# Performance work log

Measured on AMD Instinct MI355X. Metric: run time of the kernel, lower is better.

## Reference

```python
import jax, jax.numpy as jnp
import numpy as np

NUM_NODES = 100000
NODE_DIM = 64
MEM_DIM = 64
EMBED = 64   # out_channels
HEADS = 2
IN_DIM = NODE_DIM + MEM_DIM  # 128
N = 50000    # batch nodes (len(n_id))
E = 800000   # edges in local subgraph


def setup_inputs() -> dict:
    key = jax.random.key(0)
    ks = jax.random.split(key, 12)
    s = 1.0 / np.sqrt(IN_DIM)
    inp = {
        "n_id": jax.random.randint(ks[0], (N,), 0, NUM_NODES),
        "edge_index": jax.random.randint(ks[1], (2, E), 0, N),
        # non-learned TGN memory state (detached in forward)
        "memory_table": jax.random.normal(ks[2], (NUM_NODES, MEM_DIM), jnp.float32),
        # learned node embedding table
        "emb_table": jax.random.normal(ks[3], (NUM_NODES, NODE_DIM), jnp.float32),
        # TransformerConv linear layers; weights stored [in, out] so y = x @ W + b
        "Wq": jax.random.normal(ks[4], (IN_DIM, HEADS * EMBED), jnp.float32) * s,
        "bq": jnp.zeros((HEADS * EMBED,), jnp.float32),
        "Wk": jax.random.normal(ks[5], (IN_DIM, HEADS * EMBED), jnp.float32) * s,
        "bk": jnp.zeros((HEADS * EMBED,), jnp.float32),
        "Wv": jax.random.normal(ks[6], (IN_DIM, HEADS * EMBED), jnp.float32) * s,
        "bv": jnp.zeros((HEADS * EMBED,), jnp.float32),
        "Wskip": jax.random.normal(ks[7], (IN_DIM, EMBED), jnp.float32) * s,
        "bskip": jnp.zeros((EMBED,), jnp.float32),
    }
    return inp


def reference(n_id, edge_index, memory_table, emb_table, Wq, bq, Wk, bk, Wv, bv, Wskip, bskip):
    # memory lookup (detached) + embedding lookup + concat([emb, mem])
    z = jax.lax.stop_gradient(memory_table[n_id])          # [N, MEM_DIM]
    x = jnp.concatenate([emb_table[n_id], z], axis=-1)     # [N, IN_DIM]

    q = (x @ Wq + bq).reshape(N, HEADS, EMBED)
    k = (x @ Wk + bk).reshape(N, HEADS, EMBED)
    v = (x @ Wv + bv).reshape(N, HEADS, EMBED)

    src, dst = edge_index[0], edge_index[1]
    # per-edge attention score: (q_i . k_j) / sqrt(d), i = dst, j = src
    score = jnp.einsum("ehd,ehd->eh", q[dst], k[src]) / np.sqrt(EMBED)  # [E, H]
    # scatter-softmax over incoming edges of each destination node
    smax = jax.ops.segment_max(score, dst, num_segments=N)              # [N, H]
    exps = jnp.exp(score - smax[dst])                                   # [E, H]
    denom = jax.ops.segment_sum(exps, dst, num_segments=N)              # [N, H]
    alpha = exps / denom[dst]                                           # [E, H]

    msg = alpha[:, :, None] * v[src]                                    # [E, H, D]
    out = jax.ops.segment_sum(msg, dst, num_segments=N)                 # [N, H, D]
    out = out.mean(axis=1)                                              # concat=False -> mean over heads
    out = out + x @ Wskip + bskip                                       # root_weight skip
    return out
```

## Files before the change

kernel.cpp:

```cpp
#include <hip/hip_runtime.h>
#include <math.h>


typedef unsigned int uint32;
typedef unsigned short ushort16;
typedef __attribute__((ext_vector_type(8))) short short8;
typedef __attribute__((ext_vector_type(4))) float floatx4;

__device__ __forceinline__ ushort16 f2bf(float f) {
  union { float f; uint32 u; } x; x.f = f;
  uint32 r = x.u + 0x7fffu + ((x.u >> 16) & 1u);
  return (ushort16)(r >> 16);
}
__device__ __forceinline__ float bf_lo(uint32 u) {
  union { uint32 u; float f; } x; x.u = u << 16; return x.f;
}
__device__ __forceinline__ float bf_hi(uint32 u) {
  union { uint32 u; float f; } x; x.u = u & 0xffff0000u; return x.f;
}
__device__ __forceinline__ void unpack8(uint4 u, float* f) {
  f[0] = bf_lo(u.x); f[1] = bf_hi(u.x); f[2] = bf_lo(u.y); f[3] = bf_hi(u.y);
  f[4] = bf_lo(u.z); f[5] = bf_hi(u.z); f[6] = bf_lo(u.w); f[7] = bf_hi(u.w);
}
__device__ __forceinline__ short8 pack8s(float4 a, float4 b) {
  union { uint32 u[4]; short8 s; } r;
  r.u[0] = (uint32)f2bf(a.x) | ((uint32)f2bf(a.y) << 16);
  r.u[1] = (uint32)f2bf(a.z) | ((uint32)f2bf(a.w) << 16);
  r.u[2] = (uint32)f2bf(b.x) | ((uint32)f2bf(b.y) << 16);
  r.u[3] = (uint32)f2bf(b.z) | ((uint32)f2bf(b.w) << 16);
  return r.s;
}

__global__ __launch_bounds__(256) void prep_hist_kernel(
    const float* __restrict__ Wq, const float* __restrict__ bq,
    const float* __restrict__ Wk, const float* __restrict__ bk,
    const float* __restrict__ Wv, const float* __restrict__ bv,
    const float* __restrict__ Ws, const float* __restrict__ bs,
    ushort16* __restrict__ Wt, float* __restrict__ ball,
    const int* __restrict__ dstA, int E, int* __restrict__ counts) {
  int idx = blockIdx.x * 256 + threadIdx.x;
  if (idx < 448 * 128) {
    int n = idx >> 7, k = idx & 127;
    float w;
    if (n < 128)      w = Wq[k * 128 + n];
    else if (n < 256) w = Wk[k * 128 + (n - 128)];
    else if (n < 384) w = Wv[k * 128 + (n - 256)];
    else              w = Ws[k * 64 + (n - 384)];
    Wt[idx] = f2bf(w);
  }
  if (idx < 448) {
    float b;
    if (idx < 128)      b = bq[idx];
    else if (idx < 256) b = bk[idx - 128];
    else if (idx < 384) b = bv[idx - 256];
    else                b = bs[idx - 384];
    ball[idx] = b;
  }
  if (idx < E) atomicAdd(&counts[dstA[idx]], 1);
}

__global__ __launch_bounds__(256) void scan1_kernel(const int* __restrict__ counts,
                                                    int* __restrict__ offs,
                                                    int* __restrict__ bsum, int N) {
  __shared__ int s[256];
  int b = blockIdx.x, t = threadIdx.x;
  int base = b * 4096 + t * 16;
  int vals[16];
  int sum = 0;
#pragma unroll
  for (int i = 0; i < 16; ++i) {
    int idx = base + i;
    vals[i] = (idx < N) ? counts[idx] : 0;
    sum += vals[i];
  }
  s[t] = sum;
  __syncthreads();
  for (int off = 1; off < 256; off <<= 1) {
    int vv = (t >= off) ? s[t - off] : 0;
    __syncthreads();
    s[t] += vv;
    __syncthreads();
  }
  int run = (t > 0) ? s[t - 1] : 0;
#pragma unroll
  for (int i = 0; i < 16; ++i) {
    int idx = base + i;
    if (idx < N) offs[idx] = run;
    run += vals[i];
  }
  if (t == 255) bsum[b] = s[255];
}

__global__ __launch_bounds__(256) void scan3_kernel(int* __restrict__ offs,
                                                    const int* __restrict__ bsum,
                                                    int* __restrict__ cursor,
                                                    int N, int E) {
  int i = blockIdx.x * blockDim.x + threadIdx.x;
  if (i < N) {
    int blk = i >> 12;
    int add = 0;
    for (int j = 0; j < blk; ++j) add += bsum[j];
    int v = offs[i] + add;
    offs[i] = v;
    cursor[i] = v;
  }
  if (i == 0) offs[N] = E;
}

__global__ __launch_bounds__(256) void scatter_kernel(
    const int* __restrict__ srcA, const int* __restrict__ dstA, int E,
    int* __restrict__ cursor, int* __restrict__ sorted_src) {
  int e = blockIdx.x * blockDim.x + threadIdx.x;
  if (e < E) {
    int d = dstA[e];
    int p = atomicAdd(&cursor[d], 1);
    sorted_src[p] = srcA[e];
  }
}

#define LDB 136
__global__ __launch_bounds__(256) void qkv_mfma2_kernel(
    const int* __restrict__ n_id, const float* __restrict__ embtab,
    const float* __restrict__ memtab,
    const ushort16* __restrict__ Wt, const float* __restrict__ ball,
    ushort16* __restrict__ qb, ushort16* __restrict__ kb, ushort16* __restrict__ vb,
    float* __restrict__ outskip, int N) {
  __shared__ ushort16 Bs[2][64 * LDB];
  int t = threadIdx.x;
  int wave = t >> 6, lane = t & 63;
  int lrow = lane & 15, quad = lane >> 4;
  int grow = blockIdx.x * 64 + wave * 16 + lrow;
  bool rvalid = grow < N;
  int srcrow = rvalid ? n_id[grow] : 0;

  const float* embp = embtab + (size_t)srcrow * 64 + quad * 8;
  const float* memp = memtab + (size_t)srcrow * 64 + quad * 8;
  short8 af[4];
  af[0] = pack8s(*(const float4*)(embp), *(const float4*)(embp + 4));
  af[1] = pack8s(*(const float4*)(embp + 32), *(const float4*)(embp + 36));
  af[2] = pack8s(*(const float4*)(memp), *(const float4*)(memp + 4));
  af[3] = pack8s(*(const float4*)(memp + 32), *(const float4*)(memp + 36));

  int sr[4], sc[4];
  uint4 breg[4];
#pragma unroll
  for (int rep = 0; rep < 4; ++rep) {
    int idx = rep * 256 + t;
    sr[rep] = idx >> 4;
    sc[rep] = (idx & 15) * 8;
    breg[rep] = *(const uint4*)(Wt + (size_t)sr[rep] * 128 + sc[rep]);
  }
#pragma unroll
  for (int rep = 0; rep < 4; ++rep)
    *(uint4*)&Bs[0][sr[rep] * LDB + sc[rep]] = breg[rep];
  __syncthreads();

  for (int ct = 0; ct < 7; ++ct) {
    int buf = ct & 1;
    if (ct < 6) {
      const ushort16* wp = Wt + (size_t)(ct + 1) * 8192;
#pragma unroll
      for (int rep = 0; rep < 4; ++rep)
        breg[rep] = *(const uint4*)(wp + (size_t)sr[rep] * 128 + sc[rep]);
    }

    floatx4 acc[4];
#pragma unroll
    for (int j = 0; j < 4; ++j) acc[j] = (floatx4)(0.f);

#pragma unroll
    for (int kk = 0; kk < 4; ++kk) {
      int koff = kk * 32 + quad * 8;
#pragma unroll
      for (int jt = 0; jt < 4; ++jt) {
        short8 bf = *(const short8*)&Bs[buf][(jt * 16 + lrow) * LDB + koff];
        acc[jt] = __builtin_amdgcn_mfma_f32_16x16x32_bf16(bf, af[kk], acc[jt], 0, 0, 0);
      }
    }

    if (rvalid) {
      int col0 = ct * 64;
#pragma unroll
      for (int jt = 0; jt < 4; ++jt) {
        int gcol = col0 + jt * 16 + quad * 4;
        float4 bias = *(const float4*)(ball + gcol);
        float o0 = acc[jt][0] + bias.x;
        float o1 = acc[jt][1] + bias.y;
        float o2 = acc[jt][2] + bias.z;
        float o3 = acc[jt][3] + bias.w;
        if (ct < 6) {
          uint2 pk;
          pk.x = (uint32)f2bf(o0) | ((uint32)f2bf(o1) << 16);
          pk.y = (uint32)f2bf(o2) | ((uint32)f2bf(o3) << 16);
          if (ct < 2)      *(uint2*)(qb + (size_t)grow * 128 + gcol)         = pk;
          else if (ct < 4) *(uint2*)(kb + (size_t)grow * 128 + (gcol - 128)) = pk;
          else             *(uint2*)(vb + (size_t)grow * 128 + (gcol - 256)) = pk;
        } else {
          *(float4*)(outskip + (size_t)grow * 64 + (gcol - 384)) =
              make_float4(o0, o1, o2, o3);
        }
      }
    }

    if (ct < 6) {
#pragma unroll
      for (int rep = 0; rep < 4; ++rep)
        *(uint4*)&Bs[buf ^ 1][sr[rep] * LDB + sc[rep]] = breg[rep];
      __syncthreads();
    }
  }
}

#define EXPC 0.1803368801111244f
__global__ __launch_bounds__(256) void attn_kernel(
    const ushort16* __restrict__ qb, const ushort16* __restrict__ kb,
    const ushort16* __restrict__ vb, const int* __restrict__ offs,
    const int* __restrict__ ssrc, float* __restrict__ out, int N) {
  int tid = threadIdx.x;
  int wave = tid >> 6, lane = tid & 63;
  int nsub = lane >> 4;
  int l16 = lane & 15;
  int head = l16 >> 3;
  int l8 = lane & 7;
  int node = (blockIdx.x * 4 + wave) * 4 + nsub;
  bool valid = node < N;
  int nodeC = valid ? node : 0;

  int e0 = 0, e1 = 0;
  if (valid) { e0 = offs[node]; e1 = offs[node + 1]; }
  int deg = e1 - e0;
  int md = deg;
  md = max(md, __shfl_xor(md, 16));
  md = max(md, __shfl_xor(md, 32));

  int hoff = head * 64 + l8 * 8;
  float qf[8];
  {
    uint4 qu = *(const uint4*)(qb + (size_t)nodeC * 128 + hoff);
    unpack8(qu, qf);
  }

  float l = 0.f;
  float a[8];
#pragma unroll
  for (int j = 0; j < 8; ++j) a[j] = 0.f;

  uint4 k0v = make_uint4(0, 0, 0, 0), v0v = k0v, k1v = k0v, v1v = k0v;
  if (md > 0) {
    int e = e0;
    int s = (e < e1) ? ssrc[e] : 0;
    k0v = *(const uint4*)(kb + (size_t)s * 128 + hoff);
    v0v = *(const uint4*)(vb + (size_t)s * 128 + hoff);
  }
  if (md > 1) {
    int e = e0 + 1;
    int s = (e < e1) ? ssrc[e] : 0;
    k1v = *(const uint4*)(kb + (size_t)s * 128 + hoff);
    v1v = *(const uint4*)(vb + (size_t)s * 128 + hoff);
  }

  for (int i = 0; i < md; ++i) {
    uint4 kc = k0v, vc = v0v;
    k0v = k1v; v0v = v1v;
    if (i + 2 < md) {
      int e = e0 + i + 2;
      int s = (e < e1) ? ssrc[e] : 0;
      k1v = *(const uint4*)(kb + (size_t)s * 128 + hoff);
      v1v = *(const uint4*)(vb + (size_t)s * 128 + hoff);
    }
    float kf[8], vf[8];
    unpack8(kc, kf);
    unpack8(vc, vf);
    float p = qf[0] * kf[0];
#pragma unroll
    for (int j = 1; j < 8; ++j) p = fmaf(qf[j], kf[j], p);
    p += __shfl_xor(p, 1);
    p += __shfl_xor(p, 2);
    p += __shfl_xor(p, 4);
    float w = (i < deg) ? exp2f(p * EXPC) : 0.f;
    l += w;
#pragma unroll
    for (int j = 0; j < 8; ++j) a[j] = fmaf(w, vf[j], a[j]);
  }

  float inv = (l > 0.f) ? 0.5f / l : 0.f;
  float r[8];
#pragma unroll
  for (int j = 0; j < 8; ++j) r[j] = a[j] * inv;
#pragma unroll
  for (int j = 0; j < 8; ++j) r[j] += __shfl_xor(r[j], 8);

  if (valid && head == 0) {
    float* op = out + (size_t)node * 64 + l8 * 8;
    float4 c0 = *(float4*)op;
    float4 c1 = *(float4*)(op + 4);
    c0.x += r[0]; c0.y += r[1]; c0.z += r[2]; c0.w += r[3];
    c1.x += r[4]; c1.y += r[5]; c1.z += r[6]; c1.w += r[7];
    *(float4*)op = c0;
    *(float4*)(op + 4) = c1;
  }
}

extern "C" void kernel_launch(void* const* d_in, const int* in_sizes, int n_in,
                              void* d_out, int out_size, void* d_ws, size_t ws_size,
                              hipStream_t stream) {
  const int* n_id = (const int*)d_in[0];
  const int* eidx = (const int*)d_in[1];
  const float* memtab = (const float*)d_in[2];
  const float* embtab = (const float*)d_in[3];
  const float* Wq = (const float*)d_in[4];
  const float* bq = (const float*)d_in[5];
  const float* Wk = (const float*)d_in[6];
  const float* bk = (const float*)d_in[7];
  const float* Wv = (const float*)d_in[8];
  const float* bv = (const float*)d_in[9];
  const float* Wskip = (const float*)d_in[10];
  const float* bskip = (const float*)d_in[11];

  int N = in_sizes[0];
  int E = in_sizes[1] / 2;
  const int* srcA = eidx;
  const int* dstA = eidx + E;
  float* out = (float*)d_out;

  char* w = (char*)d_ws;
  ushort16* qb = (ushort16*)w; w += (size_t)N * 128 * 2;
  ushort16* kb = (ushort16*)w; w += (size_t)N * 128 * 2;
  ushort16* vb = (ushort16*)w; w += (size_t)N * 128 * 2;
  ushort16* Wt = (ushort16*)w; w += (size_t)448 * 128 * 2;
  float* ball = (float*)w;     w += (size_t)448 * 4;
  int* counts = (int*)w;       w += (size_t)N * 4;
  int* cursor = (int*)w;       w += (size_t)N * 4;
  int* offs = (int*)w;         w += (size_t)(N + 1) * 4;
  int* bsum = (int*)w;         w += (size_t)1024 * 4;
  int* ssrc = (int*)w;         w += (size_t)E * 4;

  hipMemsetAsync(counts, 0, (size_t)N * 4, stream);

  int k1_threads = (448 * 128 > E) ? 448 * 128 : E;
  prep_hist_kernel<<<(k1_threads + 255) / 256, 256, 0, stream>>>(
      Wq, bq, Wk, bk, Wv, bv, Wskip, bskip, Wt, ball, dstA, E, counts);

  int NB = (N + 4095) / 4096;
  scan1_kernel<<<NB, 256, 0, stream>>>(counts, offs, bsum, N);
  scan3_kernel<<<(N + 255) / 256, 256, 0, stream>>>(offs, bsum, cursor, N, E);

  scatter_kernel<<<(E + 255) / 256, 256, 0, stream>>>(srcA, dstA, E, cursor, ssrc);

  qkv_mfma2_kernel<<<(N + 63) / 64, 256, 0, stream>>>(
      n_id, embtab, memtab, Wt, ball, qb, kb, vb, out, N);

  attn_kernel<<<(N + 15) / 16, 256, 0, stream>>>(qb, kb, vb, offs, ssrc, out, N);
}
```

Measured before the change: 286.0 us.

## Record atomic slot in histogram, fuse scatter and offset fix-up into QKV kernel

The histogram pass now stores each edge's atomic slot, so the CSR scatter no longer needs a second atomic pass over a cursor array. The scan fix-up and scatter blocks are merged into the QKV GEMM launch as extra blocks, which removes two kernel launches and lets the scatter overlap with the matmul. The attention loop is also unrolled to handle two edges per iteration with a deeper prefetch of four. The cost is an extra E-sized pos buffer written and read, and more registers in the attention kernel.

Result: faster. 258.6 us (-9.6%).

```diff
diff --git a/kernel.cpp b/kernel.cpp
--- a/kernel.cpp
+++ b/kernel.cpp
@@ -37,7 +37,8 @@
     const float* __restrict__ Wv, const float* __restrict__ bv,
     const float* __restrict__ Ws, const float* __restrict__ bs,
     ushort16* __restrict__ Wt, float* __restrict__ ball,
-    const int* __restrict__ dstA, int E, int* __restrict__ counts) {
+    const int* __restrict__ dstA, int E, int* __restrict__ counts,
+    int* __restrict__ pos) {
   int idx = blockIdx.x * 256 + threadIdx.x;
   if (idx < 448 * 128) {
     int n = idx >> 7, k = idx & 127;
@@ -56,11 +57,11 @@
     else                b = bs[idx - 384];
     ball[idx] = b;
   }
-  if (idx < E) atomicAdd(&counts[dstA[idx]], 1);
+  if (idx < E) pos[idx] = atomicAdd(&counts[dstA[idx]], 1);
 }
 
 __global__ __launch_bounds__(256) void scan1_kernel(const int* __restrict__ counts,
-                                                    int* __restrict__ offs,
+                                                    int* __restrict__ poffs,
                                                     int* __restrict__ bsum, int N) {
   __shared__ int s[256];
   int b = blockIdx.x, t = threadIdx.x;
@@ -85,51 +86,53 @@
 #pragma unroll
   for (int i = 0; i < 16; ++i) {
     int idx = base + i;
-    if (idx < N) offs[idx] = run;
+    if (idx < N) poffs[idx] = run;
     run += vals[i];
   }
   if (t == 255) bsum[b] = s[255];
 }
 
-__global__ __launch_bounds__(256) void scan3_kernel(int* __restrict__ offs,
-                                                    const int* __restrict__ bsum,
-                                                    int* __restrict__ cursor,
-                                                    int N, int E) {
-  int i = blockIdx.x * blockDim.x + threadIdx.x;
-  if (i < N) {
-    int blk = i >> 12;
-    int add = 0;
-    for (int j = 0; j < blk; ++j) add += bsum[j];
-    int v = offs[i] + add;
-    offs[i] = v;
-    cursor[i] = v;
-  }
-  if (i == 0) offs[N] = E;
-}
-
-__global__ __launch_bounds__(256) void scatter_kernel(
-    const int* __restrict__ srcA, const int* __restrict__ dstA, int E,
-    int* __restrict__ cursor, int* __restrict__ sorted_src) {
-  int e = blockIdx.x * blockDim.x + threadIdx.x;
-  if (e < E) {
-    int d = dstA[e];
-    int p = atomicAdd(&cursor[d], 1);
-    sorted_src[p] = srcA[e];
-  }
-}
-
 #define LDB 136
-__global__ __launch_bounds__(256) void qkv_mfma2_kernel(
+__global__ __launch_bounds__(256) void fused_kernel(
     const int* __restrict__ n_id, const float* __restrict__ embtab,
     const float* __restrict__ memtab,
     const ushort16* __restrict__ Wt, const float* __restrict__ ball,
     ushort16* __restrict__ qb, ushort16* __restrict__ kb, ushort16* __restrict__ vb,
-    float* __restrict__ outskip, int N) {
+    float* __restrict__ outskip, int N,
+    const int* __restrict__ srcA, const int* __restrict__ dstA, int E,
+    const int* __restrict__ poffs, const int* __restrict__ bsum,
+    const int* __restrict__ pos, int* __restrict__ ssrc, int* __restrict__ offs,
+    int QB, int PB) {
   __shared__ ushort16 Bs[2][64 * LDB];
+  int b = blockIdx.x;
   int t = threadIdx.x;
+
+  if (b >= QB) {
+    if (b < QB + PB) {
+      int e = (b - QB) * 256 + t;
+      if (e < E) {
+        int d = dstA[e];
+        int blk = d >> 12;
+        int add = 0;
+        for (int j = 0; j < blk; ++j) add += bsum[j];
+        ssrc[poffs[d] + add + pos[e]] = srcA[e];
+      }
+    } else {
+      int i = (b - QB - PB) * 256 + t;
+      if (i < N) {
+        int blk = i >> 12;
+        int add = 0;
+        for (int j = 0; j < blk; ++j) add += bsum[j];
+        offs[i] = poffs[i] + add;
+      }
+      if (i == 0) offs[N] = E;
+    }
+    return;
+  }
+
   int wave = t >> 6, lane = t & 63;
   int lrow = lane & 15, quad = lane >> 4;
-  int grow = blockIdx.x * 64 + wave * 16 + lrow;
+  int grow = b * 64 + wave * 16 + lrow;
   bool rvalid = grow < N;
   int srcrow = rvalid ? n_id[grow] : 0;
 
@@ -245,42 +248,57 @@
 #pragma unroll
   for (int j = 0; j < 8; ++j) a[j] = 0.f;
 
-  uint4 k0v = make_uint4(0, 0, 0, 0), v0v = k0v, k1v = k0v, v1v = k0v;
-  if (md > 0) {
-    int e = e0;
+  uint4 kr[4], vr[4];
+#pragma unroll
+  for (int j = 0; j < 4; ++j) {
+    int e = e0 + j;
     int s = (e < e1) ? ssrc[e] : 0;
-    k0v = *(const uint4*)(kb + (size_t)s * 128 + hoff);
-    v0v = *(const uint4*)(vb + (size_t)s * 128 + hoff);
-  }
-  if (md > 1) {
-    int e = e0 + 1;
-    int s = (e < e1) ? ssrc[e] : 0;
-    k1v = *(const uint4*)(kb + (size_t)s * 128 + hoff);
-    v1v = *(const uint4*)(vb + (size_t)s * 128 + hoff);
-  }
-
-  for (int i = 0; i < md; ++i) {
-    uint4 kc = k0v, vc = v0v;
-    k0v = k1v; v0v = v1v;
-    if (i + 2 < md) {
-      int e = e0 + i + 2;
+    kr[j] = (j < md) ? *(const uint4*)(kb + (size_t)s * 128 + hoff) : make_uint4(0,0,0,0);
+    vr[j] = (j < md) ? *(const uint4*)(vb + (size_t)s * 128 + hoff) : make_uint4(0,0,0,0);
+  }
+
+  for (int i = 0; i < md; i += 2) {
+    uint4 kc0 = kr[0], vc0 = vr[0], kc1 = kr[1], vc1 = vr[1];
+    kr[0] = kr[2]; vr[0] = vr[2]; kr[1] = kr[3]; vr[1] = vr[3];
+    if (i + 4 < md) {
+      int e = e0 + i + 4;
       int s = (e < e1) ? ssrc[e] : 0;
-      k1v = *(const uint4*)(kb + (size_t)s * 128 + hoff);
-      v1v = *(const uint4*)(vb + (size_t)s * 128 + hoff);
-    }
-    float kf[8], vf[8];
-    unpack8(kc, kf);
-    unpack8(vc, vf);
-    float p = qf[0] * kf[0];
-#pragma unroll
-    for (int j = 1; j < 8; ++j) p = fmaf(qf[j], kf[j], p);
-    p += __shfl_xor(p, 1);
-    p += __shfl_xor(p, 2);
-    p += __shfl_xor(p, 4);
-    float w = (i < deg) ? exp2f(p * EXPC) : 0.f;
-    l += w;
-#pragma unroll
-    for (int j = 0; j < 8; ++j) a[j] = fmaf(w, vf[j], a[j]);
+      kr[2] = *(const uint4*)(kb + (size_t)s * 128 + hoff);
+      vr[2] = *(const uint4*)(vb + (size_t)s * 128 + hoff);
+    }
+    if (i + 5 < md) {
+      int e = e0 + i + 5;
+      int s = (e < e1) ? ssrc[e] : 0;
+      kr[3] = *(const uint4*)(kb + (size_t)s * 128 + hoff);
+      vr[3] = *(const uint4*)(vb + (size_t)s * 128 + hoff);
+    }
+
+    float kf0[8], vf0[8], kf1[8], vf1[8];
+    unpack8(kc0, kf0);
+    unpack8(vc0, vf0);
+    unpack8(kc1, kf1);
+    unpack8(vc1, vf1);
+    float p0 = qf[0] * kf0[0];
+    float p1 = qf[0] * kf1[0];
+#pragma unroll
+    for (int j = 1; j < 8; ++j) {
+      p0 = fmaf(qf[j], kf0[j], p0);
+      p1 = fmaf(qf[j], kf1[j], p1);
+    }
+    p0 += __shfl_xor(p0, 1);
+    p1 += __shfl_xor(p1, 1);
+    p0 += __shfl_xor(p0, 2);
+    p1 += __shfl_xor(p1, 2);
+    p0 += __shfl_xor(p0, 4);
+    p1 += __shfl_xor(p1, 4);
+    float w0 = (i < deg) ? exp2f(p0 * EXPC) : 0.f;
+    float w1 = (i + 1 < deg) ? exp2f(p1 * EXPC) : 0.f;
+    l += w0 + w1;
+#pragma unroll
+    for (int j = 0; j < 8; ++j) {
+      a[j] = fmaf(w0, vf0[j], a[j]);
+      a[j] = fmaf(w1, vf1[j], a[j]);
+    }
   }
 
   float inv = (l > 0.f) ? 0.5f / l : 0.f;
@@ -330,25 +348,27 @@
   ushort16* Wt = (ushort16*)w; w += (size_t)448 * 128 * 2;
   float* ball = (float*)w;     w += (size_t)448 * 4;
   int* counts = (int*)w;       w += (size_t)N * 4;
-  int* cursor = (int*)w;       w += (size_t)N * 4;
+  int* poffs = (int*)w;        w += (size_t)N * 4;
   int* offs = (int*)w;         w += (size_t)(N + 1) * 4;
   int* bsum = (int*)w;         w += (size_t)1024 * 4;
   int* ssrc = (int*)w;         w += (size_t)E * 4;
+  int* pos = (int*)w;          w += (size_t)E * 4;
 
   hipMemsetAsync(counts, 0, (size_t)N * 4, stream);
 
   int k1_threads = (448 * 128 > E) ? 448 * 128 : E;
   prep_hist_kernel<<<(k1_threads + 255) / 256, 256, 0, stream>>>(
-      Wq, bq, Wk, bk, Wv, bv, Wskip, bskip, Wt, ball, dstA, E, counts);
+      Wq, bq, Wk, bk, Wv, bv, Wskip, bskip, Wt, ball, dstA, E, counts, pos);
 
   int NB = (N + 4095) / 4096;
-  scan1_kernel<<<NB, 256, 0, stream>>>(counts, offs, bsum, N);
-  scan3_kernel<<<(N + 255) / 256, 256, 0, stream>>>(offs, bsum, cursor, N, E);
-
-  scatter_kernel<<<(E + 255) / 256, 256, 0, stream>>>(srcA, dstA, E, cursor, ssrc);
-
-  qkv_mfma2_kernel<<<(N + 63) / 64, 256, 0, stream>>>(
-      n_id, embtab, memtab, Wt, ball, qb, kb, vb, out, N);
+  scan1_kernel<<<NB, 256, 0, stream>>>(counts, poffs, bsum, N);
+
+  int QB = (N + 63) / 64;
+  int PB = (E + 255) / 256;
+  int FB = (N + 255) / 256;
+  fused_kernel<<<QB + PB + FB, 256, 0, stream>>>(
+      n_id, embtab, memtab, Wt, ball, qb, kb, vb, out, N,
+      srcA, dstA, E, poffs, bsum, pos, ssrc, offs, QB, PB);
 
   attn_kernel<<<(N + 15) / 16, 256, 0, stream>>>(qb, kb, vb, offs, ssrc, out, N);
 }
```

## Fuse CSR build into QKV kernel and degree-sort attention node order

Applied to the files above, without the earlier changes.

The histogram pass now records each edge's slot from its atomicAdd, so the scatter needs no second atomic cursor pass. The scan-fixup, scatter and a new degree-bucketing pass are merged into the QKV GEMM launch as extra block ranges, which cuts kernel launches and lets the independent work overlap. The attention kernel visits nodes in degree-sorted order so that the four nodes sharing a wavefront have similar edge counts and less divergence. In exchange it adds pos and norder buffers and gives up node locality when writing the output.

New measurement: 361.0 us. 26.2% more time.

```diff
diff --git a/kernel.cpp b/kernel.cpp
--- a/kernel.cpp
+++ b/kernel.cpp
@@ -37,7 +37,8 @@
     const float* __restrict__ Wv, const float* __restrict__ bv,
     const float* __restrict__ Ws, const float* __restrict__ bs,
     ushort16* __restrict__ Wt, float* __restrict__ ball,
-    const int* __restrict__ dstA, int E, int* __restrict__ counts) {
+    const int* __restrict__ dstA, int E, int* __restrict__ counts,
+    int* __restrict__ pos) {
   int idx = blockIdx.x * 256 + threadIdx.x;
   if (idx < 448 * 128) {
     int n = idx >> 7, k = idx & 127;
@@ -56,12 +57,14 @@
     else                b = bs[idx - 384];
     ball[idx] = b;
   }
-  if (idx < E) atomicAdd(&counts[dstA[idx]], 1);
+  if (idx < E) pos[idx] = atomicAdd(&counts[dstA[idx]], 1);
 }
 
 __global__ __launch_bounds__(256) void scan1_kernel(const int* __restrict__ counts,
-                                                    int* __restrict__ offs,
-                                                    int* __restrict__ bsum, int N) {
+                                                    int* __restrict__ poffs,
+                                                    int* __restrict__ bsum,
+                                                    int* __restrict__ dcnt,
+                                                    int* __restrict__ pos2, int N) {
   __shared__ int s[256];
   int b = blockIdx.x, t = threadIdx.x;
   int base = b * 4096 + t * 16;
@@ -72,6 +75,10 @@
     int idx = base + i;
     vals[i] = (idx < N) ? counts[idx] : 0;
     sum += vals[i];
+    if (idx < N) {
+      int bin = vals[i] < 63 ? vals[i] : 63;
+      pos2[idx] = atomicAdd(&dcnt[bin], 1);
+    }
   }
   s[t] = sum;
   __syncthreads();
@@ -85,51 +92,67 @@
 #pragma unroll
   for (int i = 0; i < 16; ++i) {
     int idx = base + i;
-    if (idx < N) offs[idx] = run;
+    if (idx < N) poffs[idx] = run;
     run += vals[i];
   }
   if (t == 255) bsum[b] = s[255];
 }
 
-__global__ __launch_bounds__(256) void scan3_kernel(int* __restrict__ offs,
-                                                    const int* __restrict__ bsum,
-                                                    int* __restrict__ cursor,
-                                                    int N, int E) {
-  int i = blockIdx.x * blockDim.x + threadIdx.x;
-  if (i < N) {
-    int blk = i >> 12;
-    int add = 0;
-    for (int j = 0; j < blk; ++j) add += bsum[j];
-    int v = offs[i] + add;
-    offs[i] = v;
-    cursor[i] = v;
-  }
-  if (i == 0) offs[N] = E;
-}
-
-__global__ __launch_bounds__(256) void scatter_kernel(
-    const int* __restrict__ srcA, const int* __restrict__ dstA, int E,
-    int* __restrict__ cursor, int* __restrict__ sorted_src) {
-  int e = blockIdx.x * blockDim.x + threadIdx.x;
-  if (e < E) {
-    int d = dstA[e];
-    int p = atomicAdd(&cursor[d], 1);
-    sorted_src[p] = srcA[e];
-  }
-}
-
 #define LDB 136
-__global__ __launch_bounds__(256) void qkv_mfma2_kernel(
+__global__ __launch_bounds__(256) void fused_kernel(
     const int* __restrict__ n_id, const float* __restrict__ embtab,
     const float* __restrict__ memtab,
     const ushort16* __restrict__ Wt, const float* __restrict__ ball,
     ushort16* __restrict__ qb, ushort16* __restrict__ kb, ushort16* __restrict__ vb,
-    float* __restrict__ outskip, int N) {
+    float* __restrict__ outskip, int N,
+    const int* __restrict__ srcA, const int* __restrict__ dstA, int E,
+    const int* __restrict__ poffs, const int* __restrict__ bsum,
+    const int* __restrict__ pos, int* __restrict__ ssrc, int* __restrict__ offs,
+    const int* __restrict__ counts, const int* __restrict__ dcnt,
+    const int* __restrict__ pos2, int* __restrict__ norder,
+    int QB, int PB, int FB) {
   __shared__ ushort16 Bs[2][64 * LDB];
+  int b = blockIdx.x;
   int t = threadIdx.x;
+
+  if (b >= QB) {
+    if (b < QB + PB) {
+      int e = (b - QB) * 256 + t;
+      if (e < E) {
+        int d = dstA[e];
+        int blk = d >> 12;
+        int add = 0;
+        for (int j = 0; j < blk; ++j) add += bsum[j];
+        ssrc[poffs[d] + add + pos[e]] = srcA[e];
+      }
+    } else if (b < QB + PB + FB) {
+      int i = (b - QB - PB) * 256 + t;
+      if (i < N) {
+        int blk = i >> 12;
+        int add = 0;
+        for (int j = 0; j < blk; ++j) add += bsum[j];
+        offs[i] = poffs[i] + add;
+      }
+      if (i == 0) offs[N] = E;
+    } else {
+      __shared__ int dls[64];
+      if (t < 64) dls[t] = dcnt[t];
+      __syncthreads();
+      int i = (b - QB - PB - FB) * 256 + t;
+      if (i < N) {
+        int deg = counts[i];
+        int bin = deg < 63 ? deg : 63;
+        int dbase = 0;
+        for (int j = 0; j < bin; ++j) dbase += dls[j];
+        norder[dbase + pos2[i]] = i;
+      }
+    }
+    return;
+  }
+
   int wave = t >> 6, lane = t & 63;
   int lrow = lane & 15, quad = lane >> 4;
-  int grow = blockIdx.x * 64 + wave * 16 + lrow;
+  int grow = b * 64 + wave * 16 + lrow;
   bool rvalid = grow < N;
   int srcrow = rvalid ? n_id[grow] : 0;
 
@@ -215,16 +238,17 @@
 __global__ __launch_bounds__(256) void attn_kernel(
     const ushort16* __restrict__ qb, const ushort16* __restrict__ kb,
     const ushort16* __restrict__ vb, const int* __restrict__ offs,
-    const int* __restrict__ ssrc, float* __restrict__ out, int N) {
+    const int* __restrict__ ssrc, const int* __restrict__ norder,
+    float* __restrict__ out, int N) {
   int tid = threadIdx.x;
   int wave = tid >> 6, lane = tid & 63;
   int nsub = lane >> 4;
   int l16 = lane & 15;
   int head = l16 >> 3;
   int l8 = lane & 7;
-  int node = (blockIdx.x * 4 + wave) * 4 + nsub;
-  bool valid = node < N;
-  int nodeC = valid ? node : 0;
+  int sidx = (blockIdx.x * 4 + wave) * 4 + nsub;
+  bool valid = sidx < N;
+  int node = valid ? norder[sidx] : 0;
 
   int e0 = 0, e1 = 0;
   if (valid) { e0 = offs[node]; e1 = offs[node + 1]; }
@@ -236,7 +260,7 @@
   int hoff = head * 64 + l8 * 8;
   float qf[8];
   {
-    uint4 qu = *(const uint4*)(qb + (size_t)nodeC * 128 + hoff);
+    uint4 qu = *(const uint4*)(qb + (size_t)node * 128 + hoff);
     unpack8(qu, qf);
   }
 
@@ -330,25 +354,32 @@
   ushort16* Wt = (ushort16*)w; w += (size_t)448 * 128 * 2;
   float* ball = (float*)w;     w += (size_t)448 * 4;
   int* counts = (int*)w;       w += (size_t)N * 4;
-  int* cursor = (int*)w;       w += (size_t)N * 4;
+  int* dcnt = (int*)w;         w += (size_t)64 * 4;
+  int* poffs = (int*)w;        w += (size_t)N * 4;
   int* offs = (int*)w;         w += (size_t)(N + 1) * 4;
   int* bsum = (int*)w;         w += (size_t)1024 * 4;
   int* ssrc = (int*)w;         w += (size_t)E * 4;
-
-  hipMemsetAsync(counts, 0, (size_t)N * 4, stream);
+  int* pos = (int*)w;          w += (size_t)E * 4;
+  int* pos2 = (int*)w;         w += (size_t)N * 4;
+  int* norder = (int*)w;       w += (size_t)N * 4;
+
+  hipMemsetAsync(counts, 0, (size_t)(N + 64) * 4, stream);
 
   int k1_threads = (448 * 128 > E) ? 448 * 128 : E;
   prep_hist_kernel<<<(k1_threads + 255) / 256, 256, 0, stream>>>(
-      Wq, bq, Wk, bk, Wv, bv, Wskip, bskip, Wt, ball, dstA, E, counts);
+      Wq, bq, Wk, bk, Wv, bv, Wskip, bskip, Wt, ball, dstA, E, counts, pos);
 
   int NB = (N + 4095) / 4096;
-  scan1_kernel<<<NB, 256, 0, stream>>>(counts, offs, bsum, N);
-  scan3_kernel<<<(N + 255) / 256, 256, 0, stream>>>(offs, bsum, cursor, N, E);
-
-  scatter_kernel<<<(E + 255) / 256, 256, 0, stream>>>(srcA, dstA, E, cursor, ssrc);
-
-  qkv_mfma2_kernel<<<(N + 63) / 64, 256, 0, stream>>>(
-      n_id, embtab, memtab, Wt, ball, qb, kb, vb, out, N);
-
-  attn_kernel<<<(N + 15) / 16, 256, 0, stream>>>(qb, kb, vb, offs, ssrc, out, N);
-}
+  scan1_kernel<<<NB, 256, 0, stream>>>(counts, poffs, bsum, dcnt, pos2, N);
+
+  int QB = (N + 63) / 64;
+  int PB = (E + 255) / 256;
+  int FB = (N + 255) / 256;
+  int OB = (N + 255) / 256;
+  fused_kernel<<<QB + PB + FB + OB, 256, 0, stream>>>(
+      n_id, embtab, memtab, Wt, ball, qb, kb, vb, out, N,
+      srcA, dstA, E, poffs, bsum, pos, ssrc, offs,
+      counts, dcnt, pos2, norder, QB, PB, FB);
+
+  attn_kernel<<<(N + 15) / 16, 256, 0, stream>>>(qb, kb, vb, offs, ssrc, norder, out, N);
+}
```
